# Performance work log

Hardware: AMD Instinct MI355X
Metric: run time of the kernel (lower is better)

The kernel has to match this reference:

```python
import jax, jax.numpy as jnp
import numpy as np
from jax import lax

D_H = 256      # d_hidden
D_S = 552      # d_spec
V = 148        # len(textproc.symbols)
LT = 128       # Lt_max
B = 64         # batch
ST = 800       # St_max (< max_dec_len)
MAX_DEC = 1000


def _lstm_cell(x, h, c, Wih, Whh, bih, bhh):
    # PyTorch gate order: i, f, g, o
    gates = x @ Wih.T + h @ Whh.T + bih + bhh  # [B, 4H]
    i, f, g, o = jnp.split(gates, 4, axis=-1)
    c2 = jax.nn.sigmoid(f) * c + jax.nn.sigmoid(i) * jnp.tanh(g)
    h2 = jax.nn.sigmoid(o) * jnp.tanh(c2)
    return h2, c2


def setup_inputs() -> dict:
    key = jax.random.key(0)
    ks = jax.random.split(key, 24)
    s = 0.05
    inp = {
        'token_pad': jax.random.randint(ks[0], (LT, B), 0, V),
        'token_lengths': jax.random.randint(ks[1], (B,), 1, LT + 1),
        'S_true': jax.random.normal(ks[2], (ST, B, D_S), dtype=jnp.float32),
        'emb': jax.random.normal(ks[3], (V, D_H), dtype=jnp.float32) * s,
        # encoder LSTM
        'enc_Wih': jax.random.normal(ks[4], (4 * D_H, D_H), dtype=jnp.float32) * s,
        'enc_Whh': jax.random.normal(ks[5], (4 * D_H, D_H), dtype=jnp.float32) * s,
        'enc_bih': jax.random.normal(ks[6], (4 * D_H,), dtype=jnp.float32) * s,
        'enc_bhh': jax.random.normal(ks[7], (4 * D_H,), dtype=jnp.float32) * s,
        # decoder LSTMCell
        'dec_Wih': jax.random.normal(ks[8], (4 * D_H, D_H), dtype=jnp.float32) * s,
        'dec_Whh': jax.random.normal(ks[9], (4 * D_H, D_H), dtype=jnp.float32) * s,
        'dec_bih': jax.random.normal(ks[10], (4 * D_H,), dtype=jnp.float32) * s,
        'dec_bhh': jax.random.normal(ks[11], (4 * D_H,), dtype=jnp.float32) * s,
        # spec_pre
        'pre_W': jax.random.normal(ks[12], (D_H, D_S), dtype=jnp.float32) * s,
        'pre_b': jax.random.normal(ks[13], (D_H,), dtype=jnp.float32) * s,
        # spec_post (Linear, ReLU, Linear)
        'post_W1': jax.random.normal(ks[14], (D_H, D_H), dtype=jnp.float32) * s,
        'post_b1': jax.random.normal(ks[15], (D_H,), dtype=jnp.float32) * s,
        'post_W2': jax.random.normal(ks[16], (D_S, D_H), dtype=jnp.float32) * s,
        'post_b2': jax.random.normal(ks[17], (D_S,), dtype=jnp.float32) * s,
        # stop_layer (Linear, ReLU, Linear->1)
        'stop_W1': jax.random.normal(ks[18], (D_H, D_H), dtype=jnp.float32) * s,
        'stop_b1': jax.random.normal(ks[19], (D_H,), dtype=jnp.float32) * s,
        'stop_W2': jax.random.normal(ks[20], (1, D_H), dtype=jnp.float32) * s,
        'stop_b2': jax.random.normal(ks[21], (1,), dtype=jnp.float32) * s,
    }
    return inp


def reference(token_pad, token_lengths, S_true, emb,
              enc_Wih, enc_Whh, enc_bih, enc_bhh,
              dec_Wih, dec_Whh, dec_bih, dec_bhh,
              pre_W, pre_b, post_W1, post_b1, post_W2, post_b2,
              stop_W1, stop_b1, stop_W2, stop_b2):
    # ---- encoder: embedding + masked LSTM (emulates pack_padded_sequence) ----
    token_emb = emb[token_pad]                                   # [LT, B, H]
    mask = jnp.arange(LT)[:, None] < token_lengths[None, :]      # [LT, B]

    h0 = jnp.zeros((B, D_H), dtype=token_emb.dtype)

    def enc_step(carry, xs):
        h, c = carry
        x, m = xs
        h2, c2 = _lstm_cell(x, h, c, enc_Wih, enc_Whh, enc_bih, enc_bhh)
        m = m[:, None]
        return (jnp.where(m, h2, h), jnp.where(m, c2, c)), None

    (h_n, _), _ = lax.scan(enc_step, (h0, h0), (token_emb, mask))
    enc_out = h_n                                                # [B, H]

    # ---- decoder: 1000 teacher-forced steps ----
    # F.pad S_true to max_dec_len, input at t=0 is zeros, t>0 is S_true_ext[t]
    S_in = jnp.zeros((MAX_DEC, B, D_S), dtype=S_true.dtype).at[:ST].set(S_true)
    S_in = S_in.at[0].set(0.0)

    def dec_step(carry, frame):
        h, c = carry
        x = frame @ pre_W.T + pre_b                              # spec_pre
        h, c = _lstm_cell(x, h, c, dec_Wih, dec_Whh, dec_bih, dec_bhh)
        hid = jax.nn.relu(h @ post_W1.T + post_b1)
        S_out = hid @ post_W2.T + post_b2                        # [B, D_S]
        sh = jax.nn.relu(h @ stop_W1.T + stop_b1)
        stop = (sh @ stop_W2.T + stop_b2)[:, 0]                  # [B]
        return (h, c), (S_out, stop)

    _, (S_pred, stop_logits) = lax.scan(dec_step, (enc_out, enc_out), S_in)
    return S_pred, stop_logits                                   # [1000,B,552], [1000,B]
```

## Files before the change

### kernel.cpp

```cpp
#include <hip/hip_runtime.h>

#define DH 256
#define DS 552
#define DS_PAD 576
#define NG 1024
#define LTOK 128
#define STEPS_DEC 1000
#define ST_TRUE 800
#define TOTAL_STEPS (LTOK + STEPS_DEC)
#define NREC 16
#define GRID_BLKS 128
#define NHELP (GRID_BLKS - NREC)
#define LDG 68
#define LDH 264

typedef __attribute__((ext_vector_type(8))) short bf16x8;
typedef __attribute__((ext_vector_type(4))) float f32x4;

#define OFF_FLAGS    0
#define OFF_GXD      4096
#define OFF_HPL      8192
#define OFF_WHE_HI   139264
#define OFF_WHE_LO   663552
#define OFF_WHD_HI   1187840
#define OFF_WHD_LO   1712128
#define OFF_WC_HI    2236416
#define OFF_WC_LO    3416064
#define OFF_W1_HI    4595712
#define OFF_W1_LO    4726784
#define OFF_W2_HI    4857856
#define OFF_W2_LO    5152768
#define OFF_SW1_HI   5447680
#define OFF_SW1_LO   5578752
#define OFF_EMB2     5709824
#define OFF_BCOMB    6316032
#define OFF_WCF      6320128
#define OFF_HBF      8581120
#define OFF_GX       41349120
#define WS_NEED      146206720ULL

__device__ __forceinline__ unsigned short f2bf_rn(float x) {
  unsigned u = __builtin_bit_cast(unsigned, x);
  u += 0x7fffu + ((u >> 16) & 1u);
  return (unsigned short)(u >> 16);
}
__device__ __forceinline__ float bf2f(unsigned short h) {
  unsigned u = ((unsigned)h) << 16;
  return __builtin_bit_cast(float, u);
}
__device__ __forceinline__ f32x4 mfma16(bf16x8 a, bf16x8 b, f32x4 c) {
  return __builtin_amdgcn_mfma_f32_16x16x32_bf16(a, b, c, 0, 0, 0);
}

__global__ __launch_bounds__(256) void prep_wcomb_kernel(
    const float* __restrict__ Wih, const float* __restrict__ preW,
    const float* __restrict__ pre_b, const float* __restrict__ bih,
    const float* __restrict__ bhh, float* __restrict__ WcombF,
    float* __restrict__ bcomb) {
  __shared__ float row[DH];
  __shared__ float red[256];
  int g = blockIdx.x, tid = threadIdx.x;
  row[tid] = Wih[g * DH + tid];
  __syncthreads();
  float a0 = 0.f, a1 = 0.f, a2 = 0.f;
  for (int j = 0; j < DH; ++j) {
    float wv = row[j];
    const float* pr = preW + j * DS;
    a0 += wv * pr[tid];
    a1 += wv * pr[tid + 256];
    if (tid < DS - 512) a2 += wv * pr[tid + 512];
  }
  WcombF[g * DS + tid] = a0;
  WcombF[g * DS + tid + 256] = a1;
  if (tid < DS - 512) WcombF[g * DS + tid + 512] = a2;
  red[tid] = row[tid] * pre_b[tid];
  __syncthreads();
  for (int s = 128; s > 0; s >>= 1) {
    if (tid < s) red[tid] += red[tid + s];
    __syncthreads();
  }
  if (tid == 0) bcomb[g] = red[0] + bih[g] + bhh[g];
}

__global__ __launch_bounds__(256) void prep_emb2_kernel(
    const float* __restrict__ emb, const float* __restrict__ Wih,
    const float* __restrict__ bih, const float* __restrict__ bhh,
    float* __restrict__ emb2) {
  __shared__ float erow[DH];
  int v = blockIdx.x, tid = threadIdx.x;
  erow[tid] = emb[v * DH + tid];
  __syncthreads();
  for (int c = 0; c < 4; ++c) {
    int g = c * 256 + tid;
    const float* wr = Wih + g * DH;
    float acc = 0.f;
    for (int j = 0; j < DH; ++j) acc += erow[j] * wr[j];
    emb2[v * NG + g] = acc + bih[g] + bhh[g];
  }
}

__global__ void split_bf16_kernel(const float* __restrict__ src,
                                  unsigned short* __restrict__ hi,
                                  unsigned short* __restrict__ lo,
                                  int rows, int cols, int ldo) {
  int idx = blockIdx.x * 256 + threadIdx.x;
  if (idx >= rows * cols) return;
  int r = idx / cols, c = idx - r * cols;
  float x = src[idx];
  unsigned short h = f2bf_rn(x);
  hi[r * ldo + c] = h;
  lo[r * ldo + c] = f2bf_rn(x - bf2f(h));
}

union SharedU {
  struct { float G[64 * LDG]; } rec;
  struct {
    unsigned short hid[64 * LDH];
    unsigned short sh[64 * LDH];
    float red[256];
  } post;
};

__global__ __launch_bounds__(256, 1) void mega_kernel(
    const unsigned short* __restrict__ whe_hi, const unsigned short* __restrict__ whe_lo,
    const unsigned short* __restrict__ whd_hi, const unsigned short* __restrict__ whd_lo,
    const unsigned short* __restrict__ wc_hi, const unsigned short* __restrict__ wc_lo,
    const unsigned short* __restrict__ w1_hi, const unsigned short* __restrict__ w1_lo,
    const unsigned short* __restrict__ w2_hi, const unsigned short* __restrict__ w2_lo,
    const unsigned short* __restrict__ sw1_hi, const unsigned short* __restrict__ sw1_lo,
    const float* __restrict__ emb2, const float* __restrict__ bcomb,
    const int* __restrict__ token_pad, const int* __restrict__ token_len,
    const float* __restrict__ Strue,
    const float* __restrict__ post_b1, const float* __restrict__ post_b2,
    const float* __restrict__ stop_b1, const float* __restrict__ stop_w2,
    const float* __restrict__ stop_b2,
    unsigned short* __restrict__ hpl, unsigned short* __restrict__ Hbf,
    _Float16* __restrict__ gx, unsigned* flags, unsigned* gxdone,
    float* __restrict__ outS, float* __restrict__ outStop) {
  __shared__ SharedU smem;
  int tid = threadIdx.x;
  int w = tid >> 6, lane = tid & 63, quad = lane >> 4, lrow = lane & 15;

  if (blockIdx.x < NREC) {
    int rb = blockIdx.x;
    int b = lane;
    int u0 = w * 4;
    int gub = 16 * rb + u0;
    int len = token_len[b];
    float bc[16];
#pragma unroll
    for (int i = 0; i < 4; ++i)
#pragma unroll
      for (int g = 0; g < 4; ++g) bc[i * 4 + g] = bcomb[g * 256 + gub + i];
    int grow0 = (lrow & 3) * 256 + 16 * rb + (lrow >> 2);
    bf16x8 Bh[4][8], Bl[4][8];
#pragma unroll
    for (int j = 0; j < 4; ++j)
#pragma unroll
      for (int ks = 0; ks < 8; ++ks) {
        size_t off = (size_t)(grow0 + 4 * j) * DH + ks * 32 + quad * 8;
        Bh[j][ks] = *(const bf16x8*)(whe_hi + off);
        Bl[j][ks] = *(const bf16x8*)(whe_lo + off);
      }
    float c[4] = {0.f, 0.f, 0.f, 0.f}, h[4] = {0.f, 0.f, 0.f, 0.f};
    float xc[16], xn[16];
    {
      int tok = token_pad[b];
#pragma unroll
      for (int i = 0; i < 4; ++i)
#pragma unroll
        for (int g = 0; g < 4; ++g)
          xc[i * 4 + g] = emb2[(size_t)tok * NG + g * 256 + gub + i];
    }
    int gxwm = 0;
    float* G = smem.rec.G;
    for (int S = 0; S < TOTAL_STEPS; ++S) {
      if (S == LTOK) {
#pragma unroll
        for (int j = 0; j < 4; ++j)
#pragma unroll
          for (int ks = 0; ks < 8; ++ks) {
            size_t off = (size_t)(grow0 + 4 * j) * DH + ks * 32 + quad * 8;
            Bh[j][ks] = *(const bf16x8*)(whd_hi + off);
            Bl[j][ks] = *(const bf16x8*)(whd_lo + off);
          }
#pragma unroll
        for (int i = 0; i < 4; ++i) c[i] = h[i];
      }
      int dn = S + 1 - LTOK;
      if (dn >= 1 && dn < ST_TRUE) {
        while (gxwm < dn) {
          if (__hip_atomic_load(&gxdone[gxwm + 1], __ATOMIC_RELAXED,
                                __HIP_MEMORY_SCOPE_AGENT) >= 16u)
            ++gxwm;
          else
            __builtin_amdgcn_s_sleep(1);
        }
      }
      {
        const unsigned* fp = &flags[(lane & 15) * 64];
        unsigned tgt = (unsigned)S;
        for (;;) {
          unsigned f =
              __hip_atomic_load(fp, __ATOMIC_RELAXED, __HIP_MEMORY_SCOPE_AGENT);
          if (__all(f >= tgt)) break;
          __builtin_amdgcn_s_sleep(1);
        }
      }
      __builtin_amdgcn_fence(__ATOMIC_ACQUIRE, "agent");
      if (S + 1 < LTOK) {
        int tok = token_pad[(S + 1) * 64 + b];
#pragma unroll
        for (int i = 0; i < 4; ++i)
#pragma unroll
          for (int g = 0; g < 4; ++g)
            xn[i * 4 + g] = emb2[(size_t)tok * NG + g * 256 + gub + i];
      } else if (dn >= 1 && dn < ST_TRUE) {
        const _Float16* gp = gx + ((size_t)dn * 64 + b) * NG;
#pragma unroll
        for (int i = 0; i < 4; ++i)
#pragma unroll
          for (int g = 0; g < 4; ++g)
            xn[i * 4 + g] = (float)gp[g * 256 + gub + i];
      } else {
#pragma unroll
        for (int k = 0; k < 16; ++k) xn[k] = 0.f;
      }
      const unsigned short* hb = hpl + ((S & 1) << 15);
      int arow = w * 16 + lrow;
      bf16x8 Ah[8], Al[8];
#pragma unroll
      for (int ks = 0; ks < 8; ++ks) {
        Ah[ks] = *(const bf16x8*)(hb + arow * 256 + ks * 32 + quad * 8);
        Al[ks] = *(const bf16x8*)(hb + 16384 + arow * 256 + ks * 32 + quad * 8);
      }
      f32x4 acc[4];
#pragma unroll
      for (int j = 0; j < 4; ++j) acc[j] = (f32x4){0.f, 0.f, 0.f, 0.f};
#pragma unroll
      for (int ks = 0; ks < 8; ++ks)
#pragma unroll
        for (int j = 0; j < 4; ++j) {
          acc[j] = mfma16(Ah[ks], Bh[j][ks], acc[j]);
          acc[j] = mfma16(Al[ks], Bh[j][ks], acc[j]);
          acc[j] = mfma16(Ah[ks], Bl[j][ks], acc[j]);
        }
#pragma unroll
      for (int j = 0; j < 4; ++j)
        *(f32x4*)&G[(16 * j + lrow) * LDG + 16 * w + quad * 4] = acc[j];
      __syncthreads();
      unsigned hv0, hv1, lv0, lv1;
      {
        unsigned short hhs[4], hls[4];
#pragma unroll
        for (int i = 0; i < 4; ++i) {
          float gI = G[(4 * (u0 + i) + 0) * LDG + b];
          float gF = G[(4 * (u0 + i) + 1) * LDG + b];
          float gG = G[(4 * (u0 + i) + 2) * LDG + b];
          float gO = G[(4 * (u0 + i) + 3) * LDG + b];
          if (S < LTOK) {
            gI += xc[i * 4 + 0]; gF += xc[i * 4 + 1];
            gG += xc[i * 4 + 2]; gO += xc[i * 4 + 3];
          } else {
            gI += bc[i * 4 + 0] + xc[i * 4 + 0];
            gF += bc[i * 4 + 1] + xc[i * 4 + 1];
            gG += bc[i * 4 + 2] + xc[i * 4 + 2];
            gO += bc[i * 4 + 3] + xc[i * 4 + 3];
          }
          float si = 1.f / (1.f + expf(-gI));
          float sf = 1.f / (1.f + expf(-gF));
          float so = 1.f / (1.f + expf(-gO));
          float c2 = sf * c[i] + si * tanhf(gG);
          float h2 = so * tanhf(c2);
          if (S < LTOK && S >= len) { c2 = c[i]; h2 = h[i]; }
          c[i] = c2; h[i] = h2;
          unsigned short hh = f2bf_rn(h2);
          hhs[i] = hh;
          hls[i] = f2bf_rn(h2 - bf2f(hh));
        }
        hv0 = (unsigned)hhs[0] | ((unsigned)hhs[1] << 16);
        hv1 = (unsigned)hhs[2] | ((unsigned)hhs[3] << 16);
        lv0 = (unsigned)hls[0] | ((unsigned)hls[1] << 16);
        lv1 = (unsigned)hls[2] | ((unsigned)hls[3] << 16);
      }
      unsigned short* ob = hpl + (((S & 1) ^ 1) << 15);
      *(uint2*)&ob[b * 256 + gub] = make_uint2(hv0, hv1);
      *(uint2*)&ob[16384 + b * 256 + gub] = make_uint2(lv0, lv1);
      if (S >= LTOK) {
        int d = S - LTOK;
        *(uint2*)&Hbf[((size_t)d * 64 + b) * 256 + gub] = make_uint2(hv0, hv1);
      }
#pragma unroll
      for (int k = 0; k < 16; ++k) xc[k] = xn[k];
      __syncthreads();
      if (tid == 0) {
        __builtin_amdgcn_fence(__ATOMIC_RELEASE, "agent");
        __hip_atomic_store(&flags[rb * 64], (unsigned)(S + 1), __ATOMIC_RELAXED,
                           __HIP_MEMORY_SCOPE_AGENT);
      }
    }
  } else {
    int hid0 = blockIdx.x - NREC;
    for (int item = hid0; item < 799 * 16; item += NHELP) {
      int t = 1 + (item >> 4);
      int n0 = (item & 15) << 6;
      f32x4 acc[4];
#pragma unroll
      for (int j = 0; j < 4; ++j) acc[j] = (f32x4){0.f, 0.f, 0.f, 0.f};
      for (int ks = 0; ks < 18; ++ks) {
        int kb = ks * 32 + quad * 8;
        bf16x8 ah, al;
        if (kb < DS) {
          const float* ap = Strue + ((size_t)t * 64 + w * 16 + lrow) * DS + kb;
          float4 x0 = *(const float4*)ap;
          float4 x1 = *(const float4*)(ap + 4);
          float xs[8] = {x0.x, x0.y, x0.z, x0.w, x1.x, x1.y, x1.z, x1.w};
#pragma unroll
          for (int j = 0; j < 8; ++j) {
            unsigned u = __builtin_bit_cast(unsigned, xs[j]);
            unsigned short hh = (unsigned short)(u >> 16);
            ah[j] = (short)hh;
            al[j] = (short)f2bf_rn(xs[j] - bf2f(hh));
          }
        } else {
#pragma unroll
          for (int j = 0; j < 8; ++j) { ah[j] = 0; al[j] = 0; }
        }
#pragma unroll
        for (int j = 0; j < 4; ++j) {
          int n = n0 + j * 16 + lrow;
          bf16x8 bh = *(const bf16x8*)(wc_hi + (size_t)n * DS_PAD + kb);
          bf16x8 bl = *(const bf16x8*)(wc_lo + (size_t)n * DS_PAD + kb);
          acc[j] = mfma16(ah, bh, acc[j]);
          acc[j] = mfma16(al, bh, acc[j]);
          acc[j] = mfma16(ah, bl, acc[j]);
        }
      }
#pragma unroll
      for (int j = 0; j < 4; ++j) {
        int n = n0 + j * 16 + lrow;
#pragma unroll
        for (int r = 0; r < 4; ++r)
          gx[((size_t)t * 64 + w * 16 + quad * 4 + r) * NG + n] =
              (_Float16)acc[j][r];
      }
      __syncthreads();
      if (tid == 0) {
        __builtin_amdgcn_fence(__ATOMIC_RELEASE, "agent");
        __hip_atomic_fetch_add(&gxdone[t], 1u, __ATOMIC_RELAXED,
                               __HIP_MEMORY_SCOPE_AGENT);
      }
      __syncthreads();
    }
    for (int d = hid0; d < STEPS_DEC; d += NHELP) {
      unsigned tgt = (unsigned)(LTOK + d + 1);
      {
        const unsigned* fp = &flags[(lane & 15) * 64];
        for (;;) {
          unsigned f =
              __hip_atomic_load(fp, __ATOMIC_RELAXED, __HIP_MEMORY_SCOPE_AGENT);
          if (__all(f >= tgt)) break;
          __builtin_amdgcn_s_sleep(8);
        }
      }
      __builtin_amdgcn_fence(__ATOMIC_ACQUIRE, "agent");
      bf16x8 Af[8];
#pragma unroll
      for (int ks = 0; ks < 8; ++ks)
        Af[ks] = *(const bf16x8*)(Hbf + ((size_t)d * 64 + w * 16 + lrow) * 256 +
                                  ks * 32 + quad * 8);
      {
        f32x4 a1[16];
#pragma unroll
        for (int j = 0; j < 16; ++j) a1[j] = (f32x4){0.f, 0.f, 0.f, 0.f};
        for (int ks = 0; ks < 8; ++ks) {
          int kb = ks * 32 + quad * 8;
#pragma unroll
          for (int j = 0; j < 16; ++j) {
            int n = j * 16 + lrow;
            bf16x8 bh = *(const bf16x8*)(w1_hi + (size_t)n * DH + kb);
            bf16x8 bl = *(const bf16x8*)(w1_lo + (size_t)n * DH + kb);
            a1[j] = mfma16(Af[ks], bh, a1[j]);
            a1[j] = mfma16(Af[ks], bl, a1[j]);
          }
        }
#pragma unroll
        for (int j = 0; j < 16; ++j) {
          int n = j * 16 + lrow;
          float bv = post_b1[n];
#pragma unroll
          for (int r = 0; r < 4; ++r) {
            float v = fmaxf(a1[j][r] + bv, 0.f);
            smem.post.hid[(16 * w + quad * 4 + r) * LDH + n] = f2bf_rn(v);
          }
        }
#pragma unroll
        for (int j = 0; j < 16; ++j) a1[j] = (f32x4){0.f, 0.f, 0.f, 0.f};
        for (int ks = 0; ks < 8; ++ks) {
          int kb = ks * 32 + quad * 8;
#pragma unroll
          for (int j = 0; j < 16; ++j) {
            int n = j * 16 + lrow;
            bf16x8 bh = *(const bf16x8*)(sw1_hi + (size_t)n * DH + kb);
            bf16x8 bl = *(const bf16x8*)(sw1_lo + (size_t)n * DH + kb);
            a1[j] = mfma16(Af[ks], bh, a1[j]);
            a1[j] = mfma16(Af[ks], bl, a1[j]);
          }
        }
#pragma unroll
        for (int j = 0; j < 16; ++j) {
          int n = j * 16 + lrow;
          float bv = stop_b1[n];
#pragma unroll
          for (int r = 0; r < 4; ++r) {
            float v = fmaxf(a1[j][r] + bv, 0.f);
            smem.post.sh[(16 * w + quad * 4 + r) * LDH + n] = f2bf_rn(v);
          }
        }
      }
      __syncthreads();
      {
        bf16x8 Hf[8];
#pragma unroll
        for (int ks = 0; ks < 8; ++ks)
          Hf[ks] = *(const bf16x8*)&smem.post
                        .hid[(16 * w + lrow) * LDH + ks * 32 + quad * 8];
        f32x4 a2[36];
#pragma unroll
        for (int j = 0; j < 36; ++j) a2[j] = (f32x4){0.f, 0.f, 0.f, 0.f};
        for (int ks = 0; ks < 8; ++ks) {
          int kb = ks * 32 + quad * 8;
#pragma unroll
          for (int j = 0; j < 36; ++j) {
            int n = j * 16 + lrow;
            bf16x8 bh = *(const bf16x8*)(w2_hi + (size_t)n * DH + kb);
            bf16x8 bl = *(const bf16x8*)(w2_lo + (size_t)n * DH + kb);
            a2[j] = mfma16(Hf[ks], bh, a2[j]);
            a2[j] = mfma16(Hf[ks], bl, a2[j]);
          }
        }
#pragma unroll
        for (int j = 0; j < 36; ++j) {
          int n = j * 16 + lrow;
          if (n < DS) {
            float bv = post_b2[n];
#pragma unroll
            for (int r = 0; r < 4; ++r)
              outS[((size_t)d * 64 + 16 * w + quad * 4 + r) * DS + n] =
                  a2[j][r] + bv;
          }
        }
      }
      {
        int bb = tid >> 2, kq = tid & 3;
        float a = 0.f;
        for (int kk = 0; kk < 64; kk += 8) {
          bf16x8 v = *(const bf16x8*)&smem.post.sh[bb * LDH + kq * 64 + kk];
          const float* wp = stop_w2 + kq * 64 + kk;
#pragma unroll
          for (int j = 0; j < 8; ++j) a += bf2f((unsigned short)v[j]) * wp[j];
        }
        smem.post.red[tid] = a;
      }
      __syncthreads();
      if (tid < 64)
        outStop[(size_t)d * 64 + tid] =
            smem.post.red[tid * 4] + smem.post.red[tid * 4 + 1] +
            smem.post.red[tid * 4 + 2] + smem.post.red[tid * 4 + 3] +
            stop_b2[0];
      __syncthreads();
    }
  }
}

extern "C" void kernel_launch(void* const* d_in, const int* in_sizes, int n_in,
                              void* d_out, int out_size, void* d_ws,
                              size_t ws_size, hipStream_t stream) {
  const int* token_pad = (const int*)d_in[0];
  const int* token_len = (const int*)d_in[1];
  const float* S_true = (const float*)d_in[2];
  const float* emb = (const float*)d_in[3];
  const float* enc_Wih = (const float*)d_in[4];
  const float* enc_Whh = (const float*)d_in[5];
  const float* enc_bih = (const float*)d_in[6];
  const float* enc_bhh = (const float*)d_in[7];
  const float* dec_Wih = (const float*)d_in[8];
  const float* dec_Whh = (const float*)d_in[9];
  const float* dec_bih = (const float*)d_in[10];
  const float* dec_bhh = (const float*)d_in[11];
  const float* pre_W = (const float*)d_in[12];
  const float* pre_b = (const float*)d_in[13];
  const float* post_W1 = (const float*)d_in[14];
  const float* post_b1 = (const float*)d_in[15];
  const float* post_W2 = (const float*)d_in[16];
  const float* post_b2 = (const float*)d_in[17];
  const float* stop_W1 = (const float*)d_in[18];
  const float* stop_b1 = (const float*)d_in[19];
  const float* stop_W2 = (const float*)d_in[20];
  const float* stop_b2 = (const float*)d_in[21];

  if (ws_size < WS_NEED) return;
  char* ws = (char*)d_ws;
  unsigned* flags = (unsigned*)(ws + OFF_FLAGS);
  unsigned* gxdone = (unsigned*)(ws + OFF_GXD);
  unsigned short* hpl = (unsigned short*)(ws + OFF_HPL);
  unsigned short* whe_hi = (unsigned short*)(ws + OFF_WHE_HI);
  unsigned short* whe_lo = (unsigned short*)(ws + OFF_WHE_LO);
  unsigned short* whd_hi = (unsigned short*)(ws + OFF_WHD_HI);
  unsigned short* whd_lo = (unsigned short*)(ws + OFF_WHD_LO);
  unsigned short* wc_hi = (unsigned short*)(ws + OFF_WC_HI);
  unsigned short* wc_lo = (unsigned short*)(ws + OFF_WC_LO);
  unsigned short* w1_hi = (unsigned short*)(ws + OFF_W1_HI);
  unsigned short* w1_lo = (unsigned short*)(ws + OFF_W1_LO);
  unsigned short* w2_hi = (unsigned short*)(ws + OFF_W2_HI);
  unsigned short* w2_lo = (unsigned short*)(ws + OFF_W2_LO);
  unsigned short* sw1_hi = (unsigned short*)(ws + OFF_SW1_HI);
  unsigned short* sw1_lo = (unsigned short*)(ws + OFF_SW1_LO);
  float* emb2 = (float*)(ws + OFF_EMB2);
  float* bcomb = (float*)(ws + OFF_BCOMB);
  float* WcombF = (float*)(ws + OFF_WCF);
  unsigned short* Hbf = (unsigned short*)(ws + OFF_HBF);
  _Float16* gx = (_Float16*)(ws + OFF_GX);
  float* outS = (float*)d_out;
  float* outStop = outS + (size_t)STEPS_DEC * 64 * DS;

  hipMemsetAsync(ws + OFF_FLAGS, 0, 139264, stream);
  hipMemsetAsync(ws + OFF_WC_HI, 0, 2359296, stream);
  hipMemsetAsync(ws + OFF_W2_HI, 0, 589824, stream);

  prep_wcomb_kernel<<<1024, 256, 0, stream>>>(dec_Wih, pre_W, pre_b, dec_bih,
                                              dec_bhh, WcombF, bcomb);
  prep_emb2_kernel<<<148, 256, 0, stream>>>(emb, enc_Wih, enc_bih, enc_bhh,
                                            emb2);
  split_bf16_kernel<<<(1024 * 552 + 255) / 256, 256, 0, stream>>>(
      WcombF, wc_hi, wc_lo, 1024, 552, 576);
  split_bf16_kernel<<<(1024 * 256 + 255) / 256, 256, 0, stream>>>(
      dec_Whh, whd_hi, whd_lo, 1024, 256, 256);
  split_bf16_kernel<<<(1024 * 256 + 255) / 256, 256, 0, stream>>>(
      enc_Whh, whe_hi, whe_lo, 1024, 256, 256);
  split_bf16_kernel<<<(256 * 256 + 255) / 256, 256, 0, stream>>>(
      post_W1, w1_hi, w1_lo, 256, 256, 256);
  split_bf16_kernel<<<(552 * 256 + 255) / 256, 256, 0, stream>>>(
      post_W2, w2_hi, w2_lo, 552, 256, 256);
  split_bf16_kernel<<<(256 * 256 + 255) / 256, 256, 0, stream>>>(
      stop_W1, sw1_hi, sw1_lo, 256, 256, 256);

  mega_kernel<<<GRID_BLKS, 256, 0, stream>>>(
      whe_hi, whe_lo, whd_hi, whd_lo, wc_hi, wc_lo, w1_hi, w1_lo, w2_hi, w2_lo,
      sw1_hi, sw1_lo, emb2, bcomb, token_pad, token_len, S_true, post_b1,
      post_b2, stop_b1, stop_W2, stop_b2, hpl, Hbf, gx, flags, gxdone, outS,
      outStop);
}
```

Before: 9.539 ms.

## Replace agent-scope fences with relaxed atomic data accesses and prefetch inputs before spin

New measurement: 10.43 ms. 9.3% more time.

```diff
diff --git a/kernel.cpp b/kernel.cpp
--- a/kernel.cpp
+++ b/kernel.cpp
@@ -50,6 +50,24 @@
 }
 __device__ __forceinline__ f32x4 mfma16(bf16x8 a, bf16x8 b, f32x4 c) {
   return __builtin_amdgcn_mfma_f32_16x16x32_bf16(a, b, c, 0, 0, 0);
+}
+
+__device__ __forceinline__ unsigned long long ald8(const void* p) {
+  return __hip_atomic_load((unsigned long long*)p, __ATOMIC_RELAXED,
+                           __HIP_MEMORY_SCOPE_AGENT);
+}
+__device__ __forceinline__ void ast8(void* p, unsigned long long v) {
+  __hip_atomic_store((unsigned long long*)p, v, __ATOMIC_RELAXED,
+                     __HIP_MEMORY_SCOPE_AGENT);
+}
+__device__ __forceinline__ bf16x8 ald16v(const unsigned short* p) {
+  union { unsigned long long u[2]; bf16x8 v; } t;
+  t.u[0] = ald8(p);
+  t.u[1] = ald8(p + 4);
+  return t.v;
+}
+__device__ __forceinline__ unsigned long long pack64(unsigned lo, unsigned hi) {
+  return (unsigned long long)lo | ((unsigned long long)hi << 32);
 }
 
 __global__ __launch_bounds__(256) void prep_wcomb_kernel(
@@ -167,10 +185,11 @@
     {
       int tok = token_pad[b];
 #pragma unroll
-      for (int i = 0; i < 4; ++i)
-#pragma unroll
-        for (int g = 0; g < 4; ++g)
-          xc[i * 4 + g] = emb2[(size_t)tok * NG + g * 256 + gub + i];
+      for (int g = 0; g < 4; ++g) {
+        float4 e = *(const float4*)(emb2 + (size_t)tok * NG + g * 256 + gub);
+        xc[0 * 4 + g] = e.x; xc[1 * 4 + g] = e.y;
+        xc[2 * 4 + g] = e.z; xc[3 * 4 + g] = e.w;
+      }
     }
     int gxwm = 0;
     float* G = smem.rec.G;
@@ -197,6 +216,27 @@
             __builtin_amdgcn_s_sleep(1);
         }
       }
+      if (S + 1 < LTOK) {
+        int tok = token_pad[(S + 1) * 64 + b];
+#pragma unroll
+        for (int g = 0; g < 4; ++g) {
+          float4 e = *(const float4*)(emb2 + (size_t)tok * NG + g * 256 + gub);
+          xn[0 * 4 + g] = e.x; xn[1 * 4 + g] = e.y;
+          xn[2 * 4 + g] = e.z; xn[3 * 4 + g] = e.w;
+        }
+      } else if (dn >= 1 && dn < ST_TRUE) {
+        const _Float16* gp = gx + ((size_t)dn * 64 + b) * NG;
+#pragma unroll
+        for (int g = 0; g < 4; ++g) {
+          union { unsigned long long u; _Float16 f[4]; } t;
+          t.u = ald8(gp + g * 256 + gub);
+#pragma unroll
+          for (int i = 0; i < 4; ++i) xn[i * 4 + g] = (float)t.f[i];
+        }
+      } else {
+#pragma unroll
+        for (int k = 0; k < 16; ++k) xn[k] = 0.f;
+      }
       {
         const unsigned* fp = &flags[(lane & 15) * 64];
         unsigned tgt = (unsigned)S;
@@ -207,32 +247,14 @@
           __builtin_amdgcn_s_sleep(1);
         }
       }
-      __builtin_amdgcn_fence(__ATOMIC_ACQUIRE, "agent");
-      if (S + 1 < LTOK) {
-        int tok = token_pad[(S + 1) * 64 + b];
-#pragma unroll
-        for (int i = 0; i < 4; ++i)
-#pragma unroll
-          for (int g = 0; g < 4; ++g)
-            xn[i * 4 + g] = emb2[(size_t)tok * NG + g * 256 + gub + i];
-      } else if (dn >= 1 && dn < ST_TRUE) {
-        const _Float16* gp = gx + ((size_t)dn * 64 + b) * NG;
-#pragma unroll
-        for (int i = 0; i < 4; ++i)
-#pragma unroll
-          for (int g = 0; g < 4; ++g)
-            xn[i * 4 + g] = (float)gp[g * 256 + gub + i];
-      } else {
-#pragma unroll
-        for (int k = 0; k < 16; ++k) xn[k] = 0.f;
-      }
+      asm volatile("" ::: "memory");
       const unsigned short* hb = hpl + ((S & 1) << 15);
       int arow = w * 16 + lrow;
       bf16x8 Ah[8], Al[8];
 #pragma unroll
       for (int ks = 0; ks < 8; ++ks) {
-        Ah[ks] = *(const bf16x8*)(hb + arow * 256 + ks * 32 + quad * 8);
-        Al[ks] = *(const bf16x8*)(hb + 16384 + arow * 256 + ks * 32 + quad * 8);
+        Ah[ks] = ald16v(hb + arow * 256 + ks * 32 + quad * 8);
+        Al[ks] = ald16v(hb + 16384 + arow * 256 + ks * 32 + quad * 8);
       }
       f32x4 acc[4];
 #pragma unroll
@@ -284,20 +306,18 @@
         lv1 = (unsigned)hls[2] | ((unsigned)hls[3] << 16);
       }
       unsigned short* ob = hpl + (((S & 1) ^ 1) << 15);
-      *(uint2*)&ob[b * 256 + gub] = make_uint2(hv0, hv1);
-      *(uint2*)&ob[16384 + b * 256 + gub] = make_uint2(lv0, lv1);
+      ast8(&ob[b * 256 + gub], pack64(hv0, hv1));
+      ast8(&ob[16384 + b * 256 + gub], pack64(lv0, lv1));
       if (S >= LTOK) {
         int d = S - LTOK;
-        *(uint2*)&Hbf[((size_t)d * 64 + b) * 256 + gub] = make_uint2(hv0, hv1);
+        ast8(&Hbf[((size_t)d * 64 + b) * 256 + gub], pack64(hv0, hv1));
       }
 #pragma unroll
       for (int k = 0; k < 16; ++k) xc[k] = xn[k];
       __syncthreads();
-      if (tid == 0) {
-        __builtin_amdgcn_fence(__ATOMIC_RELEASE, "agent");
+      if (tid == 0)
         __hip_atomic_store(&flags[rb * 64], (unsigned)(S + 1), __ATOMIC_RELAXED,
                            __HIP_MEMORY_SCOPE_AGENT);
-      }
     }
   } else {
     int hid0 = blockIdx.x - NREC;
@@ -363,12 +383,12 @@
           __builtin_amdgcn_s_sleep(8);
         }
       }
-      __builtin_amdgcn_fence(__ATOMIC_ACQUIRE, "agent");
+      asm volatile("" ::: "memory");
       bf16x8 Af[8];
 #pragma unroll
       for (int ks = 0; ks < 8; ++ks)
-        Af[ks] = *(const bf16x8*)(Hbf + ((size_t)d * 64 + w * 16 + lrow) * 256 +
-                                  ks * 32 + quad * 8);
+        Af[ks] = ald16v(Hbf + ((size_t)d * 64 + w * 16 + lrow) * 256 +
+                        ks * 32 + quad * 8);
       {
         f32x4 a1[16];
 #pragma unroll
```
